# Kernel tuning notes

Hardware: AMD Instinct MI355X
Metric: run time of the kernel (lower is better)

Reference implementation:

```python
import jax, jax.numpy as jnp
import numpy as np

N_WIN, P, C = 2048, 64, 256      # total windows, tokens per window (8x8 partition), channels
M_SEL, KEEP, REAL = 1536, 48, 40 # selected windows, topk tokens kept per window, real (non-padded)
H, DH = 8, 32                    # heads, dim_head
EPS = 1e-5


def _ln(x, g, b):
    mu = jnp.mean(x, axis=-1, keepdims=True)
    v = jnp.mean(jnp.square(x - mu), axis=-1, keepdims=True)
    return (x - mu) * jax.lax.rsqrt(v + EPS) * g + b


def setup_inputs() -> dict:
    key = jax.random.key(0)
    ks = jax.random.split(key, 6)
    rng = np.random.default_rng(0)
    # distinct selected windows
    index_window = jnp.asarray(np.sort(rng.choice(N_WIN, size=M_SEL, replace=False)), jnp.int32)
    # per selected window: 48 distinct token positions out of 64; first 40 real, last 8 padded
    pos = np.argsort(rng.random((M_SEL, P)), axis=1)[:, :KEEP]
    tok = np.arange(M_SEL)[:, None] * P + pos           # flat rows into (M*P, C)
    index_token = jnp.asarray(tok.reshape(-1), jnp.int32)
    asy_index = jnp.asarray(tok[:, :REAL].reshape(-1), jnp.int32)
    padding_index = jnp.asarray(tok[:, REAL:].reshape(-1), jnp.int32)
    w = lambda k, s: jax.random.normal(k, s, jnp.float32) * 0.02
    return {
        "x": jax.random.normal(ks[0], (N_WIN, P, C), jnp.float32),
        "qkv_w": w(ks[1], (C, 3 * C)), "qkv_b": jnp.zeros((3 * C,), jnp.float32),
        "proj_w": w(ks[2], (C, C)), "proj_b": jnp.zeros((C,), jnp.float32),
        "norm1_g": jnp.ones((C,), jnp.float32), "norm1_b": jnp.zeros((C,), jnp.float32),
        "norm2_g": jnp.ones((C,), jnp.float32), "norm2_b": jnp.zeros((C,), jnp.float32),
        "ls1_g": jnp.full((C,), 1e-5, jnp.float32), "ls2_g": jnp.full((C,), 1e-5, jnp.float32),
        "mlp_w1": w(ks[3], (C, 4 * C)), "mlp_b1": jnp.zeros((4 * C,), jnp.float32),
        "mlp_w2": w(ks[4], (4 * C, C)), "mlp_b2": jnp.zeros((C,), jnp.float32),
        "index_window": index_window, "index_token": index_token,
        "padding_index": padding_index, "asy_index": asy_index,
        "M": M_SEL,
    }


def reference(x, qkv_w, qkv_b, proj_w, proj_b, norm1_g, norm1_b, norm2_g, norm2_b,
              ls1_g, ls2_g, mlp_w1, mlp_b1, mlp_w2, mlp_b2,
              index_window, index_token, padding_index, asy_index, M):
    scale = DH ** -0.5
    x1 = _ln(x, norm1_g, norm1_b)                       # norm1 over all windows (N,P,C)
    X = x1
    XX = x1[index_window].reshape(-1, C)                # gather selected windows -> (M*P, C)
    XX = XX.at[asy_index].set(_ln(XX[asy_index], norm2_g, norm2_b))
    shortcut = XX[asy_index]
    xt = XX[index_token].reshape(M, KEEP, C)            # gather kept tokens per window
    qkv = (xt @ qkv_w + qkv_b).reshape(M, KEEP, H, 3 * DH).transpose(0, 2, 1, 3)
    q, k, v = jnp.split(qkv, 3, axis=-1)                # each (M,H,KEEP,DH)
    attn = jnp.einsum('mhqd,mhkd->mhqk', q, k) * scale  # (M,H,Q,K)
    # scatter scores into full map keyed by KEY token row, mask padded keys, gather back
    am = attn.transpose(0, 3, 2, 1).reshape(M * KEEP, KEEP, H)
    attn_map = jnp.zeros((M * P, KEEP, H), attn.dtype)
    attn_map = attn_map.at[index_token].set(am)
    attn_map = attn_map.at[padding_index].set(-10000.0)
    attn = attn_map[index_token].reshape(M, KEEP, KEEP, H).transpose(0, 3, 2, 1)
    attn = jax.nn.softmax(attn, axis=-1)
    out = jnp.einsum('mhqk,mhkd->mhqd', attn, v).transpose(0, 2, 1, 3).reshape(M, KEEP, C)
    out = out @ proj_w + proj_b
    XX = XX.at[index_token].set(out.reshape(-1, C))
    xa = shortcut + XX[asy_index] * ls1_g               # residual + LayerScale
    hdn = jax.nn.gelu(xa @ mlp_w1 + mlp_b1, approximate=False)
    xa = xa + (hdn @ mlp_w2 + mlp_b2) * ls2_g           # (enable_CB=False path)
    XX = XX.at[asy_index].set(xa)
    Xw = X[index_window].reshape(-1, C)
    XX = XX.at[padding_index].set(Xw[padding_index])    # restore padded rows
    X = X.at[index_window].set(XX.reshape(M, P, C))     # scatter windows back
    return X
```

## Files before the change

kernel.cpp:

```cpp
#include <hip/hip_runtime.h>

typedef __attribute__((ext_vector_type(8))) short bf16x8;
typedef __attribute__((ext_vector_type(4))) float f32x4;
typedef unsigned short u16;
typedef unsigned int u32;

#define NWIN 2048
#define P 64
#define C 256
#define MSEL 1536
#define KEEP 48
#define REAL 40
#define H 8
#define DH 32
#define MROWS (MSEL * REAL)

#define OFF_WQKVT  0
#define OFF_PROJT  196608
#define OFF_W1T    262144
#define OFF_W2T    524288
#define OFF_A      786432
#define OFF_QKV    16515072
#define OFF_ATTNO  63700992

__device__ __forceinline__ u16 f2bf(float f) {
    u32 u = __float_as_uint(f);
    u += 0x7FFF + ((u >> 16) & 1);
    return (u16)(u >> 16);
}
__device__ __forceinline__ float bf2f(u16 h) { return __uint_as_float(((u32)h) << 16); }

__global__ __launch_bounds__(256) void prep_weights(const float* __restrict__ qkv_w,
                                                    const float* __restrict__ proj_w,
                                                    const float* __restrict__ w1,
                                                    const float* __restrict__ w2,
                                                    u16* __restrict__ ws) {
    int i = blockIdx.x * 256 + threadIdx.x;
    float v; int o;
    if (i < 196608) {
        int n = i >> 8, k = i & 255; v = qkv_w[k * 768 + n]; o = OFF_WQKVT + i;
    } else if (i < 262144) {
        int j = i - 196608; int n = j >> 8, k = j & 255; v = proj_w[k * 256 + n]; o = i;
    } else if (i < 524288) {
        int j = i - 262144; int n = j >> 8, k = j & 255; v = w1[k * 1024 + n]; o = i;
    } else {
        int j = i - 524288; int n = j >> 10, k = j & 1023; v = w2[k * 256 + n]; o = i;
    }
    ws[o] = f2bf(v);
}

__global__ __launch_bounds__(256) void ln1_kernel(const float* __restrict__ x,
                                                  const float* __restrict__ g,
                                                  const float* __restrict__ b,
                                                  float* __restrict__ out) {
    int row = blockIdx.x * 4 + (threadIdx.x >> 6);
    int l = threadIdx.x & 63;
    const float4 v = *(const float4*)(x + (size_t)row * C + l * 4);
    float s = v.x + v.y + v.z + v.w;
    float q = v.x * v.x + v.y * v.y + v.z * v.z + v.w * v.w;
    #pragma unroll
    for (int m = 1; m < 64; m <<= 1) { s += __shfl_xor(s, m); q += __shfl_xor(q, m); }
    float mu = s * (1.0f / C);
    float var = q * (1.0f / C) - mu * mu;
    float rs = rsqrtf(var + 1e-5f);
    float4 gg = *(const float4*)(g + l * 4);
    float4 bb = *(const float4*)(b + l * 4);
    float4 o;
    o.x = (v.x - mu) * rs * gg.x + bb.x;
    o.y = (v.y - mu) * rs * gg.y + bb.y;
    o.z = (v.z - mu) * rs * gg.z + bb.z;
    o.w = (v.w - mu) * rs * gg.w + bb.w;
    *(float4*)(out + (size_t)row * C + l * 4) = o;
}

__global__ __launch_bounds__(256) void ln2_kernel(const float* __restrict__ ln1,
                                                  const float* __restrict__ g,
                                                  const float* __restrict__ b,
                                                  const int* __restrict__ asy,
                                                  const int* __restrict__ iwin,
                                                  u16* __restrict__ A) {
    int r = blockIdx.x * 4 + (threadIdx.x >> 6);
    int l = threadIdx.x & 63;
    int flat = asy[r];
    int m = flat >> 6, p = flat & 63;
    int w = iwin[m];
    const float4 v = *(const float4*)(ln1 + ((size_t)w * P + p) * C + l * 4);
    float s = v.x + v.y + v.z + v.w;
    float q = v.x * v.x + v.y * v.y + v.z * v.z + v.w * v.w;
    #pragma unroll
    for (int mm = 1; mm < 64; mm <<= 1) { s += __shfl_xor(s, mm); q += __shfl_xor(q, mm); }
    float mu = s * (1.0f / C);
    float var = q * (1.0f / C) - mu * mu;
    float rs = rsqrtf(var + 1e-5f);
    float4 gg = *(const float4*)(g + l * 4);
    float4 bb = *(const float4*)(b + l * 4);
    ushort4 o;
    o.x = f2bf((v.x - mu) * rs * gg.x + bb.x);
    o.y = f2bf((v.y - mu) * rs * gg.y + bb.y);
    o.z = f2bf((v.z - mu) * rs * gg.z + bb.z);
    o.w = f2bf((v.w - mu) * rs * gg.w + bb.w);
    *(ushort4*)(A + (size_t)r * C + l * 4) = o;
}

template <int N, int K, class Epi>
__global__ __launch_bounds__(256) void gemm_bt(const u16* __restrict__ A,
                                               const u16* __restrict__ B, Epi epi,
                                               int chunk) {
    constexpr int NB = N / 128;
    int bid = blockIdx.x;
    bid = (bid & 7) * chunk + (bid >> 3);
    int bm = bid / NB, bn = bid % NB;
    __shared__ u16 lA[128 * 64], lB[128 * 64];
    int t = threadIdx.x;
    int l = t & 63, w = t >> 6;
    int wr = w >> 1, wc = w & 1;
    int l15 = l & 15, g4 = l >> 4;
    int xr = l15 & 7;

    f32x4 acc[4][4];
    #pragma unroll
    for (int a = 0; a < 4; a++)
        #pragma unroll
        for (int bb = 0; bb < 4; bb++)
            #pragma unroll
            for (int i = 0; i < 4; i++) acc[a][bb][i] = 0.0f;

    int rbase = w * 32 + (l >> 3);
    int cg = (l & 7) ^ (l >> 3);
    const u16* gA = A + (size_t)(bm * 128 + rbase) * K + cg * 8;
    const u16* gB = B + (size_t)(bn * 128 + rbase) * K + cg * 8;

    for (int k0 = 0; k0 < K; k0 += 64) {
        __syncthreads();
        #pragma unroll
        for (int j = 0; j < 4; j++)
            __builtin_amdgcn_global_load_lds(
                (const __attribute__((address_space(1))) u32*)(gA + (size_t)j * 8 * K + k0),
                (__attribute__((address_space(3))) u32*)(lA + w * 2048 + j * 512), 16, 0, 0);
        #pragma unroll
        for (int j = 0; j < 4; j++)
            __builtin_amdgcn_global_load_lds(
                (const __attribute__((address_space(1))) u32*)(gB + (size_t)j * 8 * K + k0),
                (__attribute__((address_space(3))) u32*)(lB + w * 2048 + j * 512), 16, 0, 0);
        __syncthreads();
        #pragma unroll
        for (int kk = 0; kk < 2; kk++) {
            bf16x8 af[4], bfr[4];
            #pragma unroll
            for (int mt = 0; mt < 4; mt++)
                af[mt] = *(const bf16x8*)(lA + (wr * 64 + mt * 16 + l15) * 64
                                             + ((kk * 4 + g4) ^ xr) * 8);
            #pragma unroll
            for (int nt = 0; nt < 4; nt++)
                bfr[nt] = *(const bf16x8*)(lB + (wc * 64 + nt * 16 + l15) * 64
                                              + ((kk * 4 + g4) ^ xr) * 8);
            #pragma unroll
            for (int mt = 0; mt < 4; mt++)
                #pragma unroll
                for (int nt = 0; nt < 4; nt++)
                    acc[mt][nt] = __builtin_amdgcn_mfma_f32_16x16x32_bf16(af[mt], bfr[nt], acc[mt][nt], 0, 0, 0);
        }
    }
    int orow = bm * 128 + wr * 64, ocol = bn * 128 + wc * 64;
    #pragma unroll
    for (int mt = 0; mt < 4; mt++)
        #pragma unroll
        for (int nt = 0; nt < 4; nt++)
            #pragma unroll
            for (int rg = 0; rg < 4; rg++)
                epi(orow + mt * 16 + g4 * 4 + rg, ocol + nt * 16 + l15, acc[mt][nt][rg]);
}

struct EpiQKV {
    const float* bias; u16* out;
    __device__ void operator()(int r, int c, float v) const {
        out[(size_t)r * 768 + c] = f2bf(v + bias[c]);
    }
};

__global__ __launch_bounds__(256) void attn_kernel(const u16* __restrict__ QKV,
                                                   u16* __restrict__ out) {
    __shared__ u16 lds[4 * (48 * 80 + 32 * 80)];
    int m = blockIdx.x;
    int t = threadIdx.x, l = t & 63, w = t >> 6;
    int l15 = l & 15, g4 = l >> 4;
    u16* Pb = lds + w * (48 * 80 + 32 * 80);
    u16* Vt = Pb + 48 * 80;

    u32* z = (u32*)Pb;
    for (int i = l; i < (48 * 80 + 32 * 80) / 2; i += 64) z[i] = 0;

    const float scale = 0.17677669529663687f;

    for (int hh = 0; hh < 2; hh++) {
        int h = w + hh * 4;
        const u16* base = QKV + (size_t)m * REAL * 768 + h * 96;

        for (int i = l; i < REAL * 4; i += 64) {
            int kk = i >> 2, dg = i & 3;
            bf16x8 vv = *(const bf16x8*)(base + (size_t)kk * 768 + 64 + dg * 8);
            #pragma unroll
            for (int j = 0; j < 8; j++) Vt[(dg * 8 + j) * 80 + kk] = vv[j];
        }

        bf16x8 zf;
        #pragma unroll
        for (int i = 0; i < 8; i++) zf[i] = 0;
        bf16x8 qf[3], kf[3];
        #pragma unroll
        for (int mt = 0; mt < 3; mt++) {
            int q = mt * 16 + l15;
            qf[mt] = (q < REAL) ? *(const bf16x8*)(base + (size_t)q * 768 + g4 * 8) : zf;
        }
        #pragma unroll
        for (int nt = 0; nt < 3; nt++) {
            int kk = nt * 16 + l15;
            kf[nt] = (kk < REAL) ? *(const bf16x8*)(base + (size_t)kk * 768 + 32 + g4 * 8) : zf;
        }
        f32x4 s[3][3];
        #pragma unroll
        for (int a = 0; a < 3; a++)
            #pragma unroll
            for (int bb = 0; bb < 3; bb++)
                #pragma unroll
                for (int i = 0; i < 4; i++) s[a][bb][i] = 0.0f;
        #pragma unroll
        for (int mt = 0; mt < 3; mt++)
            #pragma unroll
            for (int nt = 0; nt < 3; nt++)
                s[mt][nt] = __builtin_amdgcn_mfma_f32_16x16x32_bf16(qf[mt], kf[nt], s[mt][nt], 0, 0, 0);

        #pragma unroll
        for (int mt = 0; mt < 3; mt++) {
            #pragma unroll
            for (int rg = 0; rg < 4; rg++) {
                float v0 = s[mt][0][rg] * scale;
                float v1 = s[mt][1][rg] * scale;
                float v2 = s[mt][2][rg] * scale;
                bool k2ok = (32 + l15) < REAL;
                float mx = fmaxf(fmaxf(v0, v1), k2ok ? v2 : -1e30f);
                #pragma unroll
                for (int xm = 1; xm < 16; xm <<= 1) mx = fmaxf(mx, __shfl_xor(mx, xm));
                float e0 = __expf(v0 - mx);
                float e1 = __expf(v1 - mx);
                float e2 = k2ok ? __expf(v2 - mx) : 0.0f;
                float sm = e0 + e1 + e2;
                #pragma unroll
                for (int xm = 1; xm < 16; xm <<= 1) sm += __shfl_xor(sm, xm);
                float inv = 1.0f / sm;
                int q = mt * 16 + g4 * 4 + rg;
                Pb[q * 80 + l15]      = f2bf(e0 * inv);
                Pb[q * 80 + 16 + l15] = f2bf(e1 * inv);
                Pb[q * 80 + 32 + l15] = f2bf(e2 * inv);
            }
        }

        f32x4 o[3][2];
        #pragma unroll
        for (int a = 0; a < 3; a++)
            #pragma unroll
            for (int bb = 0; bb < 2; bb++)
                #pragma unroll
                for (int i = 0; i < 4; i++) o[a][bb][i] = 0.0f;
        #pragma unroll
        for (int kt = 0; kt < 2; kt++) {
            bf16x8 pf[3], vf[2];
            #pragma unroll
            for (int mt = 0; mt < 3; mt++)
                pf[mt] = *(const bf16x8*)(Pb + (mt * 16 + l15) * 80 + kt * 32 + g4 * 8);
            #pragma unroll
            for (int nt = 0; nt < 2; nt++)
                vf[nt] = *(const bf16x8*)(Vt + (nt * 16 + l15) * 80 + kt * 32 + g4 * 8);
            #pragma unroll
            for (int mt = 0; mt < 3; mt++)
                #pragma unroll
                for (int nt = 0; nt < 2; nt++)
                    o[mt][nt] = __builtin_amdgcn_mfma_f32_16x16x32_bf16(pf[mt], vf[nt], o[mt][nt], 0, 0, 0);
        }
        #pragma unroll
        for (int mt = 0; mt < 3; mt++)
            #pragma unroll
            for (int nt = 0; nt < 2; nt++)
                #pragma unroll
                for (int rg = 0; rg < 4; rg++) {
                    int q = mt * 16 + g4 * 4 + rg;
                    if (q < REAL)
                        out[((size_t)m * REAL + q) * C + h * DH + nt * 16 + l15] = f2bf(o[mt][nt][rg]);
                }
    }
}

__global__ __launch_bounds__(256) void fused_tail(const u16* __restrict__ AttnO,
                                                  const u16* __restrict__ Abuf,
                                                  const u16* __restrict__ ProjT,
                                                  const u16* __restrict__ W1T,
                                                  const u16* __restrict__ W2T,
                                                  const float* __restrict__ proj_b,
                                                  const float* __restrict__ ls1,
                                                  const float* __restrict__ b1,
                                                  const float* __restrict__ b2,
                                                  const float* __restrict__ ls2,
                                                  const int* __restrict__ asy,
                                                  const int* __restrict__ iwin,
                                                  float* __restrict__ out) {
    __shared__ u16 Xs[64 * 264];
    __shared__ u16 Hs[64 * 136];
    int r0 = blockIdx.x * 64;
    int t = threadIdx.x, l = t & 63, w = t >> 6;
    int l15 = l & 15, g4 = l >> 4;

    #pragma unroll
    for (int i = 0; i < 8; i++) {
        int flat = i * 2048 + t * 8;
        int row = flat >> 8, col = flat & 255;
        bf16x8 v = *(const bf16x8*)(AttnO + (size_t)(r0 + row) * 256 + col);
        *(bf16x8*)(Xs + row * 264 + col) = v;
    }
    __syncthreads();

    f32x4 accp[4][4];
    #pragma unroll
    for (int a = 0; a < 4; a++)
        #pragma unroll
        for (int bb = 0; bb < 4; bb++)
            #pragma unroll
            for (int i = 0; i < 4; i++) accp[a][bb][i] = 0.0f;
    for (int k0 = 0; k0 < 256; k0 += 32) {
        bf16x8 af[4], bf[4];
        #pragma unroll
        for (int mt = 0; mt < 4; mt++)
            af[mt] = *(const bf16x8*)(Xs + (mt * 16 + l15) * 264 + k0 + g4 * 8);
        #pragma unroll
        for (int nt = 0; nt < 4; nt++)
            bf[nt] = *(const bf16x8*)(ProjT + (size_t)(w * 64 + nt * 16 + l15) * 256 + k0 + g4 * 8);
        #pragma unroll
        for (int mt = 0; mt < 4; mt++)
            #pragma unroll
            for (int nt = 0; nt < 4; nt++)
                accp[mt][nt] = __builtin_amdgcn_mfma_f32_16x16x32_bf16(af[mt], bf[nt], accp[mt][nt], 0, 0, 0);
    }
    __syncthreads();

    #pragma unroll
    for (int nt = 0; nt < 4; nt++) {
        int col = w * 64 + nt * 16 + l15;
        float pb = proj_b[col], l1 = ls1[col];
        #pragma unroll
        for (int mt = 0; mt < 4; mt++)
            #pragma unroll
            for (int rg = 0; rg < 4; rg++) {
                int row = mt * 16 + g4 * 4 + rg;
                float xa = bf2f(Abuf[(size_t)(r0 + row) * 256 + col]) + (accp[mt][nt][rg] + pb) * l1;
                Xs[row * 264 + col] = f2bf(xa);
            }
    }
    __syncthreads();

    f32x4 acco[4][4];
    #pragma unroll
    for (int a = 0; a < 4; a++)
        #pragma unroll
        for (int bb = 0; bb < 4; bb++)
            #pragma unroll
            for (int i = 0; i < 4; i++) acco[a][bb][i] = 0.0f;

    for (int kc = 0; kc < 8; kc++) {
        f32x4 acch[4][2];
        #pragma unroll
        for (int a = 0; a < 4; a++)
            #pragma unroll
            for (int bb = 0; bb < 2; bb++)
                #pragma unroll
                for (int i = 0; i < 4; i++) acch[a][bb][i] = 0.0f;
        for (int k0 = 0; k0 < 256; k0 += 32) {
            bf16x8 af[4], bf[2];
            #pragma unroll
            for (int mt = 0; mt < 4; mt++)
                af[mt] = *(const bf16x8*)(Xs + (mt * 16 + l15) * 264 + k0 + g4 * 8);
            #pragma unroll
            for (int nt = 0; nt < 2; nt++)
                bf[nt] = *(const bf16x8*)(W1T + (size_t)(kc * 128 + w * 32 + nt * 16 + l15) * 256 + k0 + g4 * 8);
            #pragma unroll
            for (int mt = 0; mt < 4; mt++)
                #pragma unroll
                for (int nt = 0; nt < 2; nt++)
                    acch[mt][nt] = __builtin_amdgcn_mfma_f32_16x16x32_bf16(af[mt], bf[nt], acch[mt][nt], 0, 0, 0);
        }
        __syncthreads();
        #pragma unroll
        for (int nt = 0; nt < 2; nt++) {
            int col = w * 32 + nt * 16 + l15;
            float bb1 = b1[kc * 128 + col];
            #pragma unroll
            for (int mt = 0; mt < 4; mt++)
                #pragma unroll
                for (int rg = 0; rg < 4; rg++) {
                    int row = mt * 16 + g4 * 4 + rg;
                    float x = acch[mt][nt][rg] + bb1;
                    float gl = 0.5f * x * (1.0f + erff(x * 0.70710678118654752f));
                    Hs[row * 136 + col] = f2bf(gl);
                }
        }
        __syncthreads();
        for (int k0 = 0; k0 < 128; k0 += 32) {
            bf16x8 af[4], bf[4];
            #pragma unroll
            for (int mt = 0; mt < 4; mt++)
                af[mt] = *(const bf16x8*)(Hs + (mt * 16 + l15) * 136 + k0 + g4 * 8);
            #pragma unroll
            for (int nt = 0; nt < 4; nt++)
                bf[nt] = *(const bf16x8*)(W2T + (size_t)(w * 64 + nt * 16 + l15) * 1024 + kc * 128 + k0 + g4 * 8);
            #pragma unroll
            for (int mt = 0; mt < 4; mt++)
                #pragma unroll
                for (int nt = 0; nt < 4; nt++)
                    acco[mt][nt] = __builtin_amdgcn_mfma_f32_16x16x32_bf16(af[mt], bf[nt], acco[mt][nt], 0, 0, 0);
        }
    }

    #pragma unroll
    for (int mt = 0; mt < 4; mt++)
        #pragma unroll
        for (int rg = 0; rg < 4; rg++) {
            int row = mt * 16 + g4 * 4 + rg;
            int flat = asy[r0 + row];
            size_t orow = ((size_t)iwin[flat >> 6] * P + (flat & 63)) * C;
            #pragma unroll
            for (int nt = 0; nt < 4; nt++) {
                int col = w * 64 + nt * 16 + l15;
                float xa = bf2f(Xs[row * 264 + col]);
                out[orow + col] = xa + (acco[mt][nt][rg] + b2[col]) * ls2[col];
            }
        }
}

extern "C" void kernel_launch(void* const* d_in, const int* in_sizes, int n_in,
                              void* d_out, int out_size, void* d_ws, size_t ws_size,
                              hipStream_t stream) {
    const float* x      = (const float*)d_in[0];
    const float* qkv_w  = (const float*)d_in[1];
    const float* qkv_b  = (const float*)d_in[2];
    const float* proj_w = (const float*)d_in[3];
    const float* proj_b = (const float*)d_in[4];
    const float* n1g    = (const float*)d_in[5];
    const float* n1b    = (const float*)d_in[6];
    const float* n2g    = (const float*)d_in[7];
    const float* n2b    = (const float*)d_in[8];
    const float* ls1    = (const float*)d_in[9];
    const float* ls2    = (const float*)d_in[10];
    const float* w1     = (const float*)d_in[11];
    const float* b1     = (const float*)d_in[12];
    const float* w2     = (const float*)d_in[13];
    const float* b2     = (const float*)d_in[14];
    const int*   iwin   = (const int*)d_in[15];
    const int*   asy    = (const int*)d_in[18];
    float* out = (float*)d_out;
    u16* ws = (u16*)d_ws;

    u16* WqkvT = ws + OFF_WQKVT;
    u16* ProjT = ws + OFF_PROJT;
    u16* W1T   = ws + OFF_W1T;
    u16* W2T   = ws + OFF_W2T;
    u16* Abuf  = ws + OFF_A;
    u16* QKV   = ws + OFF_QKV;
    u16* AttnO = ws + OFF_ATTNO;

    prep_weights<<<3072, 256, 0, stream>>>(qkv_w, proj_w, w1, w2, ws);
    ln1_kernel<<<(NWIN * P) / 4, 256, 0, stream>>>(x, n1g, n1b, out);
    ln2_kernel<<<MROWS / 4, 256, 0, stream>>>(out, n2g, n2b, asy, iwin, Abuf);
    {
        int nwg = (MROWS / 128) * 6;
        gemm_bt<768, 256, EpiQKV><<<nwg, 256, 0, stream>>>(Abuf, WqkvT, EpiQKV{qkv_b, QKV}, nwg / 8);
    }
    attn_kernel<<<MSEL, 256, 0, stream>>>(QKV, AttnO);
    fused_tail<<<MROWS / 64, 256, 0, stream>>>(AttnO, Abuf, ProjT, W1T, W2T,
                                               proj_b, ls1, b1, b2, ls2, asy, iwin, out);
}
```

Measured before the change: 561.3 us.

## Swizzle tail-kernel LDS tiles, load via global_load_lds, use tanh GELU

In the fused tail kernel, the padded LDS rows (stride 264/136) become unpadded rows addressed with an XOR swizzle on 16-byte column groups, to avoid bank conflicts without wasting shared memory. The attention-output tile is copied straight from global memory into LDS with global_load_lds instead of going through registers. The residual add of Abuf now happens in a separate coalesced vectorized pass rather than as scattered scalar reads. The exact erf GELU is replaced by the tanh approximation built on __expf, which cuts transcendental cost but drifts slightly from the reference's exact GELU.

New measurement: 627.1 us. 11.7% more time.

```diff
diff --git a/kernel.cpp b/kernel.cpp
--- a/kernel.cpp
+++ b/kernel.cpp
@@ -303,18 +303,24 @@
                                                   const int* __restrict__ asy,
                                                   const int* __restrict__ iwin,
                                                   float* __restrict__ out) {
-    __shared__ u16 Xs[64 * 264];
-    __shared__ u16 Hs[64 * 136];
+    __shared__ u16 Xs[64 * 256];
+    __shared__ u16 Hs[64 * 128];
     int r0 = blockIdx.x * 64;
     int t = threadIdx.x, l = t & 63, w = t >> 6;
     int l15 = l & 15, g4 = l >> 4;
-
-    #pragma unroll
-    for (int i = 0; i < 8; i++) {
-        int flat = i * 2048 + t * 8;
-        int row = flat >> 8, col = flat & 255;
-        bf16x8 v = *(const bf16x8*)(AttnO + (size_t)(r0 + row) * 256 + col);
-        *(bf16x8*)(Xs + row * 264 + col) = v;
+    int xr = l15 & 7;
+
+    {
+        int rr = w * 16 + (l >> 5);
+        int cg0 = l & 31;
+        #pragma unroll
+        for (int j = 0; j < 8; j++) {
+            int row = rr + j * 2;
+            int sg = cg0 ^ (row & 7);
+            __builtin_amdgcn_global_load_lds(
+                (const __attribute__((address_space(1))) u32*)(AttnO + (size_t)(r0 + row) * 256 + sg * 8),
+                (__attribute__((address_space(3))) u32*)(Xs + w * 4096 + j * 512), 16, 0, 0);
+        }
     }
     __syncthreads();
 
@@ -329,7 +335,7 @@
         bf16x8 af[4], bf[4];
         #pragma unroll
         for (int mt = 0; mt < 4; mt++)
-            af[mt] = *(const bf16x8*)(Xs + (mt * 16 + l15) * 264 + k0 + g4 * 8);
+            af[mt] = *(const bf16x8*)(Xs + (mt * 16 + l15) * 256 + (((k0 >> 3) + g4) ^ xr) * 8);
         #pragma unroll
         for (int nt = 0; nt < 4; nt++)
             bf[nt] = *(const bf16x8*)(ProjT + (size_t)(w * 64 + nt * 16 + l15) * 256 + k0 + g4 * 8);
@@ -345,14 +351,28 @@
     for (int nt = 0; nt < 4; nt++) {
         int col = w * 64 + nt * 16 + l15;
         float pb = proj_b[col], l1 = ls1[col];
+        int cg = col >> 3, ci = col & 7;
         #pragma unroll
         for (int mt = 0; mt < 4; mt++)
             #pragma unroll
             for (int rg = 0; rg < 4; rg++) {
                 int row = mt * 16 + g4 * 4 + rg;
-                float xa = bf2f(Abuf[(size_t)(r0 + row) * 256 + col]) + (accp[mt][nt][rg] + pb) * l1;
-                Xs[row * 264 + col] = f2bf(xa);
+                Xs[row * 256 + (cg ^ (row & 7)) * 8 + ci] = f2bf((accp[mt][nt][rg] + pb) * l1);
             }
+    }
+    __syncthreads();
+
+    #pragma unroll
+    for (int i = 0; i < 8; i++) {
+        int row = i * 8 + (t >> 5);
+        int cg = t & 31;
+        bf16x8 a = *(const bf16x8*)(Abuf + (size_t)(r0 + row) * 256 + cg * 8);
+        u16* px = Xs + row * 256 + (cg ^ (row & 7)) * 8;
+        bf16x8 xv = *(bf16x8*)px;
+        #pragma unroll
+        for (int j = 0; j < 8; j++)
+            xv[j] = (short)f2bf(bf2f((u16)a[j]) + bf2f((u16)xv[j]));
+        *(bf16x8*)px = xv;
     }
     __syncthreads();
 
@@ -376,7 +396,7 @@
             bf16x8 af[4], bf[2];
             #pragma unroll
             for (int mt = 0; mt < 4; mt++)
-                af[mt] = *(const bf16x8*)(Xs + (mt * 16 + l15) * 264 + k0 + g4 * 8);
+                af[mt] = *(const bf16x8*)(Xs + (mt * 16 + l15) * 256 + (((k0 >> 3) + g4) ^ xr) * 8);
             #pragma unroll
             for (int nt = 0; nt < 2; nt++)
                 bf[nt] = *(const bf16x8*)(W1T + (size_t)(kc * 128 + w * 32 + nt * 16 + l15) * 256 + k0 + g4 * 8);
@@ -391,14 +411,17 @@
         for (int nt = 0; nt < 2; nt++) {
             int col = w * 32 + nt * 16 + l15;
             float bb1 = b1[kc * 128 + col];
+            int cg = col >> 3, ci = col & 7;
             #pragma unroll
             for (int mt = 0; mt < 4; mt++)
                 #pragma unroll
                 for (int rg = 0; rg < 4; rg++) {
                     int row = mt * 16 + g4 * 4 + rg;
                     float x = acch[mt][nt][rg] + bb1;
-                    float gl = 0.5f * x * (1.0f + erff(x * 0.70710678118654752f));
-                    Hs[row * 136 + col] = f2bf(gl);
+                    float u = 0.7978845608f * (x + 0.044715f * x * x * x);
+                    float e = __expf(2.0f * u);
+                    float gl = x - x / (e + 1.0f);
+                    Hs[row * 128 + (cg ^ (row & 7)) * 8 + ci] = f2bf(gl);
                 }
         }
         __syncthreads();
@@ -406,7 +429,7 @@
             bf16x8 af[4], bf[4];
             #pragma unroll
             for (int mt = 0; mt < 4; mt++)
-                af[mt] = *(const bf16x8*)(Hs + (mt * 16 + l15) * 136 + k0 + g4 * 8);
+                af[mt] = *(const bf16x8*)(Hs + (mt * 16 + l15) * 128 + (((k0 >> 3) + g4) ^ xr) * 8);
             #pragma unroll
             for (int nt = 0; nt < 4; nt++)
                 bf[nt] = *(const bf16x8*)(W2T + (size_t)(w * 64 + nt * 16 + l15) * 1024 + kc * 128 + k0 + g4 * 8);
@@ -428,7 +451,7 @@
             #pragma unroll
             for (int nt = 0; nt < 4; nt++) {
                 int col = w * 64 + nt * 16 + l15;
-                float xa = bf2f(Xs[row * 264 + col]);
+                float xa = bf2f(Xs[row * 256 + ((col >> 3) ^ (row & 7)) * 8 + (col & 7)]);
                 out[orow + col] = xa + (acco[mt][nt][rg] + b2[col]) * ls2[col];
             }
         }
```
